# Kernel tuning notes

Hardware: AMD Instinct MI355X
Metric: run time of the kernel (lower is better)

## Reference

```python
import jax, jax.numpy as jnp
import numpy as np

K = 16  # number of neighbors (excluding self)


def setup_inputs() -> dict:
    key = jax.random.key(0)
    k0, k1, k2, k3, k4 = jax.random.split(key, 5)
    B, C, N, Cout = 8, 64, 4096, 64
    x = jax.random.normal(k0, (B, C, N), dtype=jnp.float32)
    s = 1.0 / np.sqrt(C).astype(np.float32)
    W1 = jax.random.normal(k1, (Cout, C), dtype=jnp.float32) * s
    b1 = jax.random.normal(k2, (Cout,), dtype=jnp.float32) * 0.01
    W2 = jax.random.normal(k3, (Cout, C), dtype=jnp.float32) * s
    b2 = jax.random.normal(k4, (Cout,), dtype=jnp.float32) * 0.01
    return {"x": x, "W1": W1, "b1": b1, "W2": W2, "b2": b2}


def _knn_idx(xt):
    # xt: [B, N, C]; squared-euclidean self-KNN, drop self (first / smallest dist)
    sq = jnp.sum(xt * xt, axis=-1)                              # [B, N]
    dist = sq[:, :, None] + sq[:, None, :] - 2.0 * jnp.einsum('bnc,bmc->bnm', xt, xt)
    _, idx = jax.lax.top_k(-dist, K + 1)                        # [B, N, K+1]
    return idx[:, :, 1:]                                        # [B, N, K]


def reference(x, W1, b1, W2, b2):
    # x: [B, C, N]
    xt = jnp.transpose(x, (0, 2, 1))                            # [B, N, C]
    idx = _knn_idx(xt)                                          # [B, N, K]
    # gather neighbors: nb[b,n,k,c] = xt[b, idx[b,n,k], c]
    nb = jax.vmap(lambda xb, ib: xb[ib])(xt, idx)               # [B, N, K, C]
    diff = nb - xt[:, :, None, :]                               # [B, N, K, C]
    message = jnp.einsum('bnkc,oc->bnko', diff, W1) + b1        # conv1 (1x1)
    x_center = jnp.einsum('bnc,oc->bno', xt, W2) + b2           # conv2 (1x1)
    edge = jax.nn.relu(x_center[:, :, None, :] + message)       # [B, N, K, Cout]
    y = jnp.max(edge, axis=2)                                   # [B, N, Cout]
    return jnp.transpose(y, (0, 2, 1))[:, :, None, :]           # [B, Cout, 1, N]
```

## Files before the change

### kernel.cpp

```cpp
#include <hip/hip_runtime.h>
#include <hip/hip_bf16.h>
#include <cstdint>

#define NB    8
#define NPTS  4096
#define NQ    4
#define NT    64
#define PROW  64
#define SENT  0xFF000000u

typedef __attribute__((ext_vector_type(8))) short bf16x8;
typedef __attribute__((ext_vector_type(4))) float f32x4;

__global__ __launch_bounds__(256) void k_prep(const float* __restrict__ x,
                                              float* __restrict__ xt,
                                              __hip_bfloat16* __restrict__ xh,
                                              __hip_bfloat16* __restrict__ xl,
                                              float* __restrict__ sq,
                                              float* __restrict__ sqn) {
  __shared__ float tile[64][65];
  const int b  = blockIdx.y;
  const int n0 = blockIdx.x * 64;
  const int t  = threadIdx.x;
#pragma unroll
  for (int i = 0; i < 16; ++i) {
    int lin = i * 256 + t;
    int c = lin >> 6, j = lin & 63;
    tile[j][c] = x[(size_t)b * 64 * NPTS + (size_t)c * NPTS + n0 + j];
  }
  __syncthreads();
#pragma unroll
  for (int i = 0; i < 16; ++i) {
    int lin = i * 256 + t;
    int j = lin >> 6, c = lin & 63;
    float v = tile[j][c];
    size_t o = ((size_t)b * NPTS + n0 + j) * 64 + c;
    xt[o] = v;
    __hip_bfloat16 h = __float2bfloat16(v);
    xh[o] = h;
    xl[o] = __float2bfloat16(v - __bfloat162float(h));
  }
  if (t < 64) {
    float s = 0.f;
#pragma unroll
    for (int c = 0; c < 64; ++c) { float v = tile[t][c]; s = fmaf(v, v, s); }
    sq [b * NPTS + t + n0] = s;
    sqn[b * NPTS + t + n0] = 0.5f * s;
  }
}

__global__ __launch_bounds__(256) void k_gsplit(const float* __restrict__ W1,
                                                const float* __restrict__ b1,
                                                const float* __restrict__ W2,
                                                const float* __restrict__ b2,
                                                __hip_bfloat16* __restrict__ gh,
                                                __hip_bfloat16* __restrict__ gl,
                                                float* __restrict__ bb) {
  const int t = threadIdx.x;
#pragma unroll 1
  for (int i = t; i < 128 * 64; i += 256) {
    int o = i >> 6, c = i & 63;
    float g = (o < 64) ? W1[o * 64 + c]
                       : (W2[(o - 64) * 64 + c] - W1[(o - 64) * 64 + c]);
    __hip_bfloat16 h = __float2bfloat16(g);
    gh[i] = h;
    gl[i] = __float2bfloat16(g - __bfloat162float(h));
  }
  if (t < 64) bb[t] = b1[t] + b2[t];
}

struct Frag { bf16x8 h0, h1; f32x4 sv; };

__global__ __launch_bounds__(256, 4) void k_knn(const __hip_bfloat16* __restrict__ xh,
                                                const float* __restrict__ sqn,
                                                unsigned* __restrict__ part) {
  __shared__ unsigned bufu[17 * 256];

  const int tid  = threadIdx.x;
  const int w    = tid >> 6;
  const int lane = tid & 63;
  const int quad = lane >> 4, l15 = lane & 15;
  const int rb   = blockIdx.x;
  const int q    = blockIdx.y;
  const int b    = blockIdx.z;
  const size_t xbase = (size_t)b * NPTS * 64;
  const int c0   = q * 1024;
  const int nrow = rb * 64 + w * 16 + l15;

  const __hip_bfloat16* ph = xh + xbase + (size_t)nrow * 64 + quad * 8;
  bf16x8 rh0 = *(const bf16x8*)(ph);
  bf16x8 rh1 = *(const bf16x8*)(ph + 32);
  rh0 = rh0 ^ (short)0x8000;
  rh1 = rh1 ^ (short)0x8000;
  const float srh = sqn[b * NPTS + nrow];

  unsigned D[16];
#pragma unroll
  for (int i = 0; i < 16; ++i) D[i] = SENT;
  unsigned thr = SENT | 0xFFFu;
  int cnt = 0;

  auto ldfrag = [&](int t) -> Frag {
    Frag f;
    const __hip_bfloat16* ah = xh + xbase + (size_t)(c0 + t * 16 + l15) * 64 + quad * 8;
    f.h0 = *(const bf16x8*)(ah);
    f.h1 = *(const bf16x8*)(ah + 32);
    f.sv = *(const f32x4*)(sqn + b * NPTS + c0 + t * 16 + quad * 4);
    return f;
  };

  auto flush = [&]() {
    unsigned E[16];
#pragma unroll
    for (int j = 0; j < 16; ++j) E[j] = bufu[j * 256 + tid];
#pragma unroll
    for (int j = 0; j < 16; ++j) E[j] = (j < cnt) ? E[j] : 0xFFFFFFFFu;
#pragma unroll
    for (int k = 2; k <= 16; k <<= 1)
#pragma unroll
      for (int j = k >> 1; j > 0; j >>= 1)
#pragma unroll
        for (int i = 0; i < 16; ++i) {
          int l = i ^ j;
          if (l > i) {
            unsigned lo = min(E[i], E[l]), hi = max(E[i], E[l]);
            bool up = ((i & k) == 0);
            E[i] = up ? lo : hi;
            E[l] = up ? hi : lo;
          }
        }
    unsigned T[16];
#pragma unroll
    for (int i = 0; i < 16; ++i) T[i] = min(D[i], E[15 - i]);
#pragma unroll
    for (int j = 8; j > 0; j >>= 1)
#pragma unroll
      for (int i = 0; i < 16; ++i) {
        int l = i ^ j;
        if (l > i) {
          unsigned lo = min(T[i], T[l]);
          T[l] = max(T[i], T[l]);
          T[i] = lo;
        }
      }
#pragma unroll
    for (int i = 0; i < 16; ++i) D[i] = T[i];
    cnt = 0;
    thr = D[15] | 0xFFFu;
  };

  auto ins = [&](float s, int m) {
    unsigned u = __float_as_uint(s);
    bool pass = (u <= thr);
    int slot = pass ? cnt : 16;
    bufu[slot * 256 + tid] = (u & 0xFFFFF000u) | (unsigned)m;
    cnt += pass;
  };

  auto compute2 = [&](const Frag& fa, const Frag& fb, int tbase) {
    f32x4 m1 = fa.sv, m3 = fb.sv;
#pragma unroll
    for (int i = 0; i < 4; ++i) { m1[i] += srh; m3[i] += srh; }
    f32x4 z = { 0.f, 0.f, 0.f, 0.f };
    f32x4 m2 = z, m4 = z;
    m1 = __builtin_amdgcn_mfma_f32_16x16x32_bf16(fa.h0, rh0, m1, 0, 0, 0);
    m2 = __builtin_amdgcn_mfma_f32_16x16x32_bf16(fa.h1, rh1, m2, 0, 0, 0);
    m3 = __builtin_amdgcn_mfma_f32_16x16x32_bf16(fb.h0, rh0, m3, 0, 0, 0);
    m4 = __builtin_amdgcn_mfma_f32_16x16x32_bf16(fb.h1, rh1, m4, 0, 0, 0);
    const int cb = c0 + tbase * 16 + quad * 4;
#pragma unroll
    for (int i = 0; i < 4; ++i) ins(m1[i] + m2[i], cb + i);
#pragma unroll
    for (int i = 0; i < 4; ++i) ins(m3[i] + m4[i], cb + 16 + i);
  };

  Frag a0 = ldfrag(0), a1 = ldfrag(1);
#pragma unroll 1
  for (int it = 0; it < 16; ++it) {
    const int t4 = it * 4;
    Frag b0 = ldfrag((t4 + 2) & 63), b1 = ldfrag((t4 + 3) & 63);
    compute2(a0, a1, t4);
    if (__any(cnt >= 9)) flush();
    a0 = ldfrag((t4 + 4) & 63);
    a1 = ldfrag((t4 + 5) & 63);
    compute2(b0, b1, t4 + 2);
    if (__any(cnt >= 9)) flush();
  }
  flush();

#pragma unroll
  for (int rd = 0; rd < 2; ++rd) {
    const int dx = (rd == 0) ? 16 : 32;
    unsigned Bx[16], T[16];
#pragma unroll
    for (int i = 0; i < 16; ++i) Bx[i] = (unsigned)__shfl_xor((int)D[i], dx);
#pragma unroll
    for (int i = 0; i < 16; ++i) T[i] = min(D[i], Bx[15 - i]);
#pragma unroll
    for (int j = 8; j > 0; j >>= 1)
#pragma unroll
      for (int i = 0; i < 16; ++i) {
        int l = i ^ j;
        if (l > i) {
          unsigned lo = min(T[i], T[l]);
          T[l] = max(T[i], T[l]);
          T[i] = lo;
        }
      }
#pragma unroll
    for (int i = 0; i < 16; ++i) D[i] = T[i];
  }
  if (quad == 0) {
    const size_t base = (size_t)(b * NPTS + nrow) * PROW + (size_t)q * 16;
#pragma unroll
    for (int i = 0; i < 16; ++i) part[base + i] = D[i];
  }
}

__global__ __launch_bounds__(256) void k_merge(const unsigned* __restrict__ part,
                                               unsigned short* __restrict__ cand) {
  const int row  = blockIdx.x * 4 + (threadIdx.x >> 6);
  const int lane = threadIdx.x & 63;
  const unsigned val = part[(size_t)row * PROW + lane];
  int rk = 0;
#pragma unroll
  for (int j = 0; j < 64; ++j) {
    unsigned vj = (unsigned)__shfl((int)val, j);
    rk += (vj < val);
  }
  if (rk < 20) cand[(size_t)row * 20 + rk] = (unsigned short)(val & 0xFFFu);
}

__global__ __launch_bounds__(256) void k_rerank(const float* __restrict__ xt,
                                                const float* __restrict__ sq,
                                                const unsigned short* __restrict__ cand,
                                                int* __restrict__ knn) {
  const int row = blockIdx.x * 8 + (threadIdx.x >> 5);
  const int c   = threadIdx.x & 31;
  const int b   = row >> 12;
  const int m   = cand[(size_t)row * 20 + (c < 20 ? c : 0)];
  const float4* cr = (const float4*)(xt + (size_t)row * 64);
  const float4* mr = (const float4*)(xt + ((size_t)(b << 12) + m) * 64);
  float d = 0.f;
#pragma unroll
  for (int j = 0; j < 16; ++j) {
    float4 a = cr[j], v = mr[j];
    d = fmaf(a.x, v.x, d); d = fmaf(a.y, v.y, d);
    d = fmaf(a.z, v.z, d); d = fmaf(a.w, v.w, d);
  }
  float key = sq[(b << 12) + m] - 2.f * d;
  if (m == (row & 4095)) key = 1e30f;
  int rk = 0;
#pragma unroll
  for (int j = 0; j < 20; ++j) {
    float kj = __shfl(key, j, 32);
    int   mj = __shfl(m, j, 32);
    rk += (kj < key) || ((kj == key) && (mj < m));
  }
  if (c < 20 && rk < 16) knn[(size_t)row * 16 + rk] = m;
}

__global__ __launch_bounds__(256) void k_pq(const __hip_bfloat16* __restrict__ xh,
                                            const __hip_bfloat16* __restrict__ xl,
                                            const __hip_bfloat16* __restrict__ gh,
                                            const __hip_bfloat16* __restrict__ gl,
                                            const float* __restrict__ bb,
                                            float* __restrict__ P,
                                            float* __restrict__ Q) {
  const int tid  = threadIdx.x;
  const int w    = tid >> 6;
  const int lane = tid & 63;
  const int quad = lane >> 4, l15 = lane & 15;
  const int row0 = blockIdx.x * 64 + w * 16;

  const __hip_bfloat16* pa = xh + (size_t)(row0 + l15) * 64 + quad * 8;
  const __hip_bfloat16* pb = xl + (size_t)(row0 + l15) * 64 + quad * 8;
  const bf16x8 ah0 = *(const bf16x8*)(pa);
  const bf16x8 ah1 = *(const bf16x8*)(pa + 32);
  const bf16x8 al0 = *(const bf16x8*)(pb);
  const bf16x8 al1 = *(const bf16x8*)(pb + 32);

#pragma unroll
  for (int ct = 0; ct < 8; ++ct) {
    const __hip_bfloat16* qh = gh + (size_t)(ct * 16 + l15) * 64 + quad * 8;
    const __hip_bfloat16* ql = gl + (size_t)(ct * 16 + l15) * 64 + quad * 8;
    bf16x8 bh0 = *(const bf16x8*)(qh);
    bf16x8 bh1 = *(const bf16x8*)(qh + 32);
    bf16x8 bl0 = *(const bf16x8*)(ql);
    bf16x8 bl1 = *(const bf16x8*)(ql + 32);
    f32x4 m1 = { 0.f, 0.f, 0.f, 0.f };
    f32x4 m2 = m1, m3 = m1, m4 = m1, m5 = m1, m6 = m1;
    m1 = __builtin_amdgcn_mfma_f32_16x16x32_bf16(ah0, bh0, m1, 0, 0, 0);
    m2 = __builtin_amdgcn_mfma_f32_16x16x32_bf16(ah1, bh1, m2, 0, 0, 0);
    m3 = __builtin_amdgcn_mfma_f32_16x16x32_bf16(ah0, bl0, m3, 0, 0, 0);
    m4 = __builtin_amdgcn_mfma_f32_16x16x32_bf16(ah1, bl1, m4, 0, 0, 0);
    m5 = __builtin_amdgcn_mfma_f32_16x16x32_bf16(al0, bh0, m5, 0, 0, 0);
    m6 = __builtin_amdgcn_mfma_f32_16x16x32_bf16(al1, bh1, m6, 0, 0, 0);
    if (ct < 4) {
#pragma unroll
      for (int i = 0; i < 4; ++i) {
        float s = ((m1[i] + m2[i]) + (m3[i] + m4[i])) + (m5[i] + m6[i]);
        P[(size_t)(row0 + quad * 4 + i) * 64 + ct * 16 + l15] = s;
      }
    } else {
      const float bq = bb[(ct - 4) * 16 + l15];
#pragma unroll
      for (int i = 0; i < 4; ++i) {
        float s = ((m1[i] + m2[i]) + (m3[i] + m4[i])) + (m5[i] + m6[i]);
        Q[(size_t)(row0 + quad * 4 + i) * 64 + (ct - 4) * 16 + l15] = s + bq;
      }
    }
  }
}

__global__ __launch_bounds__(256) void k_out(const float* __restrict__ P,
                                             const float* __restrict__ Q,
                                             const int* __restrict__ knn,
                                             float* __restrict__ out) {
  __shared__ float tile[64][65];
  const int b    = blockIdx.y;
  const int n0   = blockIdx.x * 64;
  const int wave = threadIdx.x >> 6;
  const int lane = threadIdx.x & 63;
  for (int i = 0; i < 16; ++i) {
    const int nl = wave * 16 + i;
    const int gn = b * NPTS + n0 + nl;
    float acc = -1e30f;
    const float qv = Q[(size_t)gn * 64 + lane];
    const int* id = knn + (size_t)gn * 16;
#pragma unroll
    for (int k = 0; k < 16; ++k) {
      int m = id[k];
      float p = P[((size_t)b * NPTS + m) * 64 + lane];
      acc = fmaxf(acc, qv + p);
    }
    tile[nl][lane] = fmaxf(acc, 0.f);
  }
  __syncthreads();
#pragma unroll
  for (int i = 0; i < 16; ++i) {
    const int o = i * 4 + wave;
    out[((size_t)b * 64 + o) * NPTS + n0 + lane] = tile[lane][o];
  }
}

extern "C" void kernel_launch(void* const* d_in, const int* in_sizes, int n_in,
                              void* d_out, int out_size, void* d_ws, size_t ws_size,
                              hipStream_t stream) {
  const float* x  = (const float*)d_in[0];
  const float* W1 = (const float*)d_in[1];
  const float* b1 = (const float*)d_in[2];
  const float* W2 = (const float*)d_in[3];
  const float* b2 = (const float*)d_in[4];
  float* out = (float*)d_out;

  float* ws = (float*)d_ws;
  const size_t NPT_ALL = (size_t)NB * NPTS;
  float*          XT   = ws;
  float*          SQ   = XT + NPT_ALL * 64;
  __hip_bfloat16* XH   = (__hip_bfloat16*)(SQ + NPT_ALL);
  __hip_bfloat16* XL   = XH + NPT_ALL * 64;
  unsigned*       PART = (unsigned*)(XL + NPT_ALL * 64);
  unsigned short* CAND = (unsigned short*)(PART + NPT_ALL * PROW);
  int*            KNN  = (int*)(CAND + NPT_ALL * 20);
  __hip_bfloat16* GH   = (__hip_bfloat16*)(KNN + NPT_ALL * 16);
  __hip_bfloat16* GL   = GH + 128 * 64;
  float*          BB   = (float*)(GL + 128 * 64);
  float*          SQN  = BB + 64;
  float*          Pm   = (float*)PART;
  float*          Qm   = (float*)XH;

  k_prep  <<<dim3(NPTS / 64, NB), 256, 0, stream>>>(x, XT, XH, XL, SQ, SQN);
  k_gsplit<<<dim3(1), 256, 0, stream>>>(W1, b1, W2, b2, GH, GL, BB);
  k_knn   <<<dim3(64, NQ, NB), 256, 0, stream>>>(XH, SQN, PART);
  k_merge <<<dim3(NPT_ALL / 4), 256, 0, stream>>>(PART, CAND);
  k_rerank<<<dim3(NPT_ALL / 8), 256, 0, stream>>>(XT, SQ, CAND, KNN);
  k_pq    <<<dim3(NPT_ALL / 64), 256, 0, stream>>>(XH, XL, GH, GL, BB, Pm, Qm);
  k_out   <<<dim3(NPTS / 64, NB), 256, 0, stream>>>(Pm, Qm, KNN, out);
}
```

Measured before the change: 331.7 us.

## Fuse weight split into prep, merge+rerank into one kernel, chain MFMA accumulators

```diff
diff --git a/kernel.cpp b/kernel.cpp
--- a/kernel.cpp
+++ b/kernel.cpp
@@ -13,15 +13,36 @@
 typedef __attribute__((ext_vector_type(4))) float f32x4;
 
 __global__ __launch_bounds__(256) void k_prep(const float* __restrict__ x,
+                                              const float* __restrict__ W1,
+                                              const float* __restrict__ b1,
+                                              const float* __restrict__ W2,
+                                              const float* __restrict__ b2,
                                               float* __restrict__ xt,
                                               __hip_bfloat16* __restrict__ xh,
                                               __hip_bfloat16* __restrict__ xl,
                                               float* __restrict__ sq,
-                                              float* __restrict__ sqn) {
+                                              float* __restrict__ sqn,
+                                              __hip_bfloat16* __restrict__ gh,
+                                              __hip_bfloat16* __restrict__ gl,
+                                              float* __restrict__ bb) {
+  const int t = threadIdx.x;
+  if (blockIdx.x == 64) {
+    if (blockIdx.y != 0) return;
+#pragma unroll 1
+    for (int i = t; i < 128 * 64; i += 256) {
+      int o = i >> 6, c = i & 63;
+      float g = (o < 64) ? W1[o * 64 + c]
+                         : (W2[(o - 64) * 64 + c] - W1[(o - 64) * 64 + c]);
+      __hip_bfloat16 h = __float2bfloat16(g);
+      gh[i] = h;
+      gl[i] = __float2bfloat16(g - __bfloat162float(h));
+    }
+    if (t < 64) bb[t] = b1[t] + b2[t];
+    return;
+  }
   __shared__ float tile[64][65];
   const int b  = blockIdx.y;
   const int n0 = blockIdx.x * 64;
-  const int t  = threadIdx.x;
 #pragma unroll
   for (int i = 0; i < 16; ++i) {
     int lin = i * 256 + t;
@@ -49,29 +70,9 @@
   }
 }
 
-__global__ __launch_bounds__(256) void k_gsplit(const float* __restrict__ W1,
-                                                const float* __restrict__ b1,
-                                                const float* __restrict__ W2,
-                                                const float* __restrict__ b2,
-                                                __hip_bfloat16* __restrict__ gh,
-                                                __hip_bfloat16* __restrict__ gl,
-                                                float* __restrict__ bb) {
-  const int t = threadIdx.x;
-#pragma unroll 1
-  for (int i = t; i < 128 * 64; i += 256) {
-    int o = i >> 6, c = i & 63;
-    float g = (o < 64) ? W1[o * 64 + c]
-                       : (W2[(o - 64) * 64 + c] - W1[(o - 64) * 64 + c]);
-    __hip_bfloat16 h = __float2bfloat16(g);
-    gh[i] = h;
-    gl[i] = __float2bfloat16(g - __bfloat162float(h));
-  }
-  if (t < 64) bb[t] = b1[t] + b2[t];
-}
-
 struct Frag { bf16x8 h0, h1; f32x4 sv; };
 
-__global__ __launch_bounds__(256, 4) void k_knn(const __hip_bfloat16* __restrict__ xh,
+__global__ __launch_bounds__(256, 8) void k_knn(const __hip_bfloat16* __restrict__ xh,
                                                 const float* __restrict__ sqn,
                                                 unsigned* __restrict__ part) {
   __shared__ unsigned bufu[17 * 256];
@@ -161,28 +162,27 @@
     f32x4 m1 = fa.sv, m3 = fb.sv;
 #pragma unroll
     for (int i = 0; i < 4; ++i) { m1[i] += srh; m3[i] += srh; }
-    f32x4 z = { 0.f, 0.f, 0.f, 0.f };
-    f32x4 m2 = z, m4 = z;
     m1 = __builtin_amdgcn_mfma_f32_16x16x32_bf16(fa.h0, rh0, m1, 0, 0, 0);
-    m2 = __builtin_amdgcn_mfma_f32_16x16x32_bf16(fa.h1, rh1, m2, 0, 0, 0);
     m3 = __builtin_amdgcn_mfma_f32_16x16x32_bf16(fb.h0, rh0, m3, 0, 0, 0);
-    m4 = __builtin_amdgcn_mfma_f32_16x16x32_bf16(fb.h1, rh1, m4, 0, 0, 0);
+    m1 = __builtin_amdgcn_mfma_f32_16x16x32_bf16(fa.h1, rh1, m1, 0, 0, 0);
+    m3 = __builtin_amdgcn_mfma_f32_16x16x32_bf16(fb.h1, rh1, m3, 0, 0, 0);
     const int cb = c0 + tbase * 16 + quad * 4;
 #pragma unroll
-    for (int i = 0; i < 4; ++i) ins(m1[i] + m2[i], cb + i);
-#pragma unroll
-    for (int i = 0; i < 4; ++i) ins(m3[i] + m4[i], cb + 16 + i);
+    for (int i = 0; i < 4; ++i) ins(m1[i], cb + i);
+#pragma unroll
+    for (int i = 0; i < 4; ++i) ins(m3[i], cb + 16 + i);
   };
 
   Frag a0 = ldfrag(0), a1 = ldfrag(1);
 #pragma unroll 1
   for (int it = 0; it < 16; ++it) {
     const int t4 = it * 4;
-    Frag b0 = ldfrag((t4 + 2) & 63), b1 = ldfrag((t4 + 3) & 63);
+    Frag b0 = ldfrag(t4 + 2), b1 = ldfrag(t4 + 3);
     compute2(a0, a1, t4);
     if (__any(cnt >= 9)) flush();
-    a0 = ldfrag((t4 + 4) & 63);
-    a1 = ldfrag((t4 + 5) & 63);
+    const int tn = (t4 + 4 < NT) ? t4 + 4 : 62;
+    a0 = ldfrag(tn);
+    a1 = ldfrag(tn + 1);
     compute2(b0, b1, t4 + 2);
     if (__any(cnt >= 9)) flush();
   }
@@ -217,28 +217,29 @@
   }
 }
 
-__global__ __launch_bounds__(256) void k_merge(const unsigned* __restrict__ part,
-                                               unsigned short* __restrict__ cand) {
-  const int row  = blockIdx.x * 4 + (threadIdx.x >> 6);
-  const int lane = threadIdx.x & 63;
-  const unsigned val = part[(size_t)row * PROW + lane];
-  int rk = 0;
-#pragma unroll
-  for (int j = 0; j < 64; ++j) {
-    unsigned vj = (unsigned)__shfl((int)val, j);
-    rk += (vj < val);
-  }
-  if (rk < 20) cand[(size_t)row * 20 + rk] = (unsigned short)(val & 0xFFFu);
-}
-
-__global__ __launch_bounds__(256) void k_rerank(const float* __restrict__ xt,
-                                                const float* __restrict__ sq,
-                                                const unsigned short* __restrict__ cand,
-                                                int* __restrict__ knn) {
-  const int row = blockIdx.x * 8 + (threadIdx.x >> 5);
+__global__ __launch_bounds__(256) void k_mr(const unsigned* __restrict__ part,
+                                            const float* __restrict__ xt,
+                                            const float* __restrict__ sq,
+                                            int* __restrict__ knn) {
+  __shared__ unsigned short lc[8][20];
+  const int g   = threadIdx.x >> 5;
   const int c   = threadIdx.x & 31;
-  const int b   = row >> 12;
-  const int m   = cand[(size_t)row * 20 + (c < 20 ? c : 0)];
+  const int row = blockIdx.x * 8 + g;
+  const unsigned v0 = part[(size_t)row * PROW + c];
+  const unsigned v1 = part[(size_t)row * PROW + 32 + c];
+  int r0 = 0, r1 = 0;
+#pragma unroll
+  for (int j = 0; j < 32; ++j) {
+    unsigned a = (unsigned)__shfl((int)v0, j, 32);
+    unsigned d = (unsigned)__shfl((int)v1, j, 32);
+    r0 += (a < v0) + (d < v0);
+    r1 += (a < v1) + (d < v1);
+  }
+  if (r0 < 20) lc[g][r0] = (unsigned short)(v0 & 0xFFFu);
+  if (r1 < 20) lc[g][r1] = (unsigned short)(v1 & 0xFFFu);
+  __syncthreads();
+  const int b = row >> 12;
+  const int m = lc[g][c < 20 ? c : 0];
   const float4* cr = (const float4*)(xt + (size_t)row * 64);
   const float4* mr = (const float4*)(xt + ((size_t)(b << 12) + m) * 64);
   float d = 0.f;
@@ -358,23 +359,22 @@
   const size_t NPT_ALL = (size_t)NB * NPTS;
   float*          XT   = ws;
   float*          SQ   = XT + NPT_ALL * 64;
-  __hip_bfloat16* XH   = (__hip_bfloat16*)(SQ + NPT_ALL);
+  float*          SQN  = SQ + NPT_ALL;
+  __hip_bfloat16* XH   = (__hip_bfloat16*)(SQN + NPT_ALL);
   __hip_bfloat16* XL   = XH + NPT_ALL * 64;
   unsigned*       PART = (unsigned*)(XL + NPT_ALL * 64);
-  unsigned short* CAND = (unsigned short*)(PART + NPT_ALL * PROW);
-  int*            KNN  = (int*)(CAND + NPT_ALL * 20);
+  int*            KNN  = (int*)(PART + NPT_ALL * PROW);
   __hip_bfloat16* GH   = (__hip_bfloat16*)(KNN + NPT_ALL * 16);
   __hip_bfloat16* GL   = GH + 128 * 64;
   float*          BB   = (float*)(GL + 128 * 64);
-  float*          SQN  = BB + 64;
   float*          Pm   = (float*)PART;
-  float*          Qm   = (float*)XH;
-
-  k_prep  <<<dim3(NPTS / 64, NB), 256, 0, stream>>>(x, XT, XH, XL, SQ, SQN);
-  k_gsplit<<<dim3(1), 256, 0, stream>>>(W1, b1, W2, b2, GH, GL, BB);
-  k_knn   <<<dim3(64, NQ, NB), 256, 0, stream>>>(XH, SQN, PART);
-  k_merge <<<dim3(NPT_ALL / 4), 256, 0, stream>>>(PART, CAND);
-  k_rerank<<<dim3(NPT_ALL / 8), 256, 0, stream>>>(XT, SQ, CAND, KNN);
-  k_pq    <<<dim3(NPT_ALL / 64), 256, 0, stream>>>(XH, XL, GH, GL, BB, Pm, Qm);
-  k_out   <<<dim3(NPTS / 64, NB), 256, 0, stream>>>(Pm, Qm, KNN, out);
-}
+  float*          Qm   = XT;
+
+  k_prep <<<dim3(NPTS / 64 + 1, NB), 256, 0, stream>>>(x, W1, b1, W2, b2,
+                                                       XT, XH, XL, SQ, SQN,
+                                                       GH, GL, BB);
+  k_knn  <<<dim3(64, NQ, NB), 256, 0, stream>>>(XH, SQN, PART);
+  k_mr   <<<dim3(NPT_ALL / 8), 256, 0, stream>>>(PART, XT, SQ, KNN);
+  k_pq   <<<dim3(NPT_ALL / 64), 256, 0, stream>>>(XH, XL, GH, GL, BB, Pm, Qm);
+  k_out  <<<dim3(NPTS / 64, NB), 256, 0, stream>>>(Pm, Qm, KNN, out);
+}
```

Measured after the change: 503.9 us. 1.52x slower.
